# Performance work log

Measured on AMD Instinct MI355X. Metric: run time of the kernel, lower is better.

The kernel has to match this reference:

```python
import jax, jax.numpy as jnp
import numpy as np
from jax.scipy.linalg import expm

DIM = 2048        # state dimension (init arg `dim`)
M_STEPS = 8192    # kernel length (init arg `timestamp`)
DELTA = 0.01      # ZOH step size (init arg `delta`)
STAB = 1e-3       # stabilizer added to A before inversion (matches torch code)


def setup_inputs() -> dict:
    key = jax.random.key(0)
    k1, k2, k3 = jax.random.split(key, 3)
    # Match the torch init scaling so matrix_exp/inv stay well-conditioned.
    A = jnp.eye(DIM, dtype=jnp.float32) * -0.01 \
        + jax.random.normal(k1, (DIM, DIM), dtype=jnp.float32) * 0.001
    B = jax.random.normal(k2, (DIM, 1), dtype=jnp.float32) * 0.01
    C = jax.random.normal(k3, (1, DIM), dtype=jnp.float32) * 0.01
    return {"A": A, "B": B, "C": C, "M": M_STEPS}


def reference(A, B, C, M):
    dim = A.shape[0]
    I = jnp.eye(dim, dtype=A.dtype)
    # --- ZOH discretization (torch._zoh_discretize) ---
    A_bar = expm(DELTA * A)                         # [dim, dim]
    A_inv = jnp.linalg.inv(A + STAB * I)            # [dim, dim]
    B_bar = A_inv @ (A_bar - I) @ (DELTA * B)       # [dim, 1]

    # --- kernel power iteration (torch._compute_K_bar) ---
    # K[t] = C @ A_bar^t @ B_bar. Since B_bar is a vector, the serial
    # matrix-power loop reduces to M sequential matvecs (same math).
    def step(x, _):
        term = (C @ x)[0, 0]        # scalar K_t
        return A_bar @ x, term      # advance state: A_bar^{t+1} B_bar

    _, terms = jax.lax.scan(step, B_bar, None, length=M)  # [M]
    K_bar = terms[::-1][None, :]    # flip along time, shape [1, M]
    return K_bar
```

## Files before the change

kernel.cpp:

```cpp
#include <hip/hip_runtime.h>
#include <hip/hip_bf16.h>


#define DIMN 2048
#define MSTEPS 8192
#define RSPLIT 91
#define NN ((size_t)DIMN * DIMN)
#define NBLK 32
#define ALD 36
#define GJP 65
#define TBM 128

typedef short short8 __attribute__((ext_vector_type(8)));
typedef float f32x4 __attribute__((ext_vector_type(4)));

__device__ inline void split1(float x, unsigned short& h, unsigned short& l)
{
  __hip_bfloat16 b = __float2bfloat16(x);
  h = *reinterpret_cast<unsigned short*>(&b);
  float r = x - __bfloat162float(b);
  __hip_bfloat16 b2 = __float2bfloat16(r);
  l = *reinterpret_cast<unsigned short*>(&b2);
}

__global__ __launch_bounds__(256)
void k_combine4(float* out,
                const float* i1, float c1, const float* i2, float c2,
                const float* i3, float c3, const float* i4, float c4,
                float dval)
{
  const int total = DIMN * DIMN;
  for (int idx = blockIdx.x * 256 + threadIdx.x; idx < total; idx += gridDim.x * 256) {
    float v = 0.f;
    if (i1) v = fmaf(c1, i1[idx], v);
    if (i2) v = fmaf(c2, i2[idx], v);
    if (i3) v = fmaf(c3, i3[idx], v);
    if (i4) v = fmaf(c4, i4[idx], v);
    if ((idx >> 11) == (idx & 2047)) v += dval;
    out[idx] = v;
  }
}

__global__ __launch_bounds__(256)
void k_fill64(const float* __restrict__ A, double* __restrict__ M)
{
  const int total = DIMN * DIMN;
  for (int idx = blockIdx.x * 256 + threadIdx.x; idx < total; idx += gridDim.x * 256) {
    double v = (double)A[idx];
    if ((idx >> 11) == (idx & 2047)) v += 1e-3;
    M[idx] = v;
  }
}

__global__ __launch_bounds__(256)
void k_split(const float* __restrict__ in, unsigned short* __restrict__ hi,
             unsigned short* __restrict__ lo)
{
  const int i4 = blockIdx.x * 256 + threadIdx.x;
  const float4 v = ((const float4*)in)[i4];
  ushort4 h, l;
  split1(v.x, h.x, l.x); split1(v.y, h.y, l.y);
  split1(v.z, h.z, l.z); split1(v.w, h.w, l.w);
  ((ushort4*)hi)[i4] = h;
  ((ushort4*)lo)[i4] = l;
}

__global__ __launch_bounds__(256)
void k_splitboth(const float* __restrict__ in,
                 unsigned short* __restrict__ hi, unsigned short* __restrict__ lo,
                 unsigned short* __restrict__ hiT, unsigned short* __restrict__ loT)
{
  __shared__ float t[32][33];
  const int bx = blockIdx.x * 32, by = blockIdx.y * 32;
  const int lx = threadIdx.x, ly = threadIdx.y;
  for (int dy = 0; dy < 32; dy += 8) {
    const size_t o = (size_t)(by + ly + dy) * DIMN + bx + lx;
    const float v = in[o];
    t[ly + dy][lx] = v;
    unsigned short h, l;
    split1(v, h, l);
    hi[o] = h; lo[o] = l;
  }
  __syncthreads();
  for (int dy = 0; dy < 32; dy += 8) {
    const size_t o = (size_t)(bx + ly + dy) * DIMN + by + lx;
    unsigned short h, l;
    split1(t[lx][ly + dy], h, l);
    hiT[o] = h; loT[o] = l;
  }
}

__global__ __launch_bounds__(256)
void k_combsplitT(const float* __restrict__ i1, float c1,
                  const float* __restrict__ i2, float c2,
                  unsigned short* __restrict__ hiT, unsigned short* __restrict__ loT)
{
  __shared__ float t[32][33];
  const int bx = blockIdx.x * 32, by = blockIdx.y * 32;
  const int lx = threadIdx.x, ly = threadIdx.y;
  for (int dy = 0; dy < 32; dy += 8) {
    const size_t o = (size_t)(by + ly + dy) * DIMN + bx + lx;
    t[ly + dy][lx] = fmaf(c1, i1[o], c2 * i2[o]);
  }
  __syncthreads();
  for (int dy = 0; dy < 32; dy += 8) {
    const size_t o = (size_t)(bx + ly + dy) * DIMN + by + lx;
    unsigned short h, l;
    split1(t[lx][ly + dy], h, l);
    hiT[o] = h; loT[o] = l;
  }
}

__global__ __launch_bounds__(256)
void k_gemm3(const unsigned short* __restrict__ Ahg, const unsigned short* __restrict__ Alg,
             const unsigned short* __restrict__ Bhg, const unsigned short* __restrict__ Blg,
             float* __restrict__ C, float alpha,
             const float* E1, float c1, const float* E2, float c2)
{
  __shared__ unsigned short sAh[128 * ALD];
  __shared__ unsigned short sAl[128 * ALD];
  __shared__ unsigned short sBh[128 * ALD];
  __shared__ unsigned short sBl[128 * ALD];
  const int tid = threadIdx.x;
  const int wid = tid >> 6, lane = tid & 63;
  const int lr = lane & 15, lg = lane >> 4;
  const int wm = wid >> 1, wn = wid & 1;
  const int bid0 = blockIdx.y * 16 + blockIdx.x;
  const int bids = (bid0 & 7) * 32 + (bid0 >> 3);
  const int brow = (bids >> 4) * 128, bcol = (bids & 15) * 128;
  const int sr = tid >> 1, sh = (tid & 1) * 16;

  const unsigned short* gAh = Ahg + (size_t)(brow + sr) * DIMN + sh;
  const unsigned short* gAl = Alg + (size_t)(brow + sr) * DIMN + sh;
  const unsigned short* gBh = Bhg + (size_t)(bcol + sr) * DIMN + sh;
  const unsigned short* gBl = Blg + (size_t)(bcol + sr) * DIMN + sh;

  f32x4 acc[4][4];
#pragma unroll
  for (int mf = 0; mf < 4; ++mf)
#pragma unroll
    for (int nf = 0; nf < 4; ++nf) acc[mf][nf] = (f32x4){0.f, 0.f, 0.f, 0.f};

  uint4 pa0 = *(const uint4*)gAh;      uint4 pa1 = *(const uint4*)(gAh + 8);
  uint4 pb0 = *(const uint4*)gAl;      uint4 pb1 = *(const uint4*)(gAl + 8);
  uint4 pc0 = *(const uint4*)gBh;      uint4 pc1 = *(const uint4*)(gBh + 8);
  uint4 pd0 = *(const uint4*)gBl;      uint4 pd1 = *(const uint4*)(gBl + 8);

  const int nk = DIMN / 32;
  for (int kt = 0; kt < nk; ++kt) {
    *(uint4*)&sAh[sr * ALD + sh] = pa0;  *(uint4*)&sAh[sr * ALD + sh + 8] = pa1;
    *(uint4*)&sAl[sr * ALD + sh] = pb0;  *(uint4*)&sAl[sr * ALD + sh + 8] = pb1;
    *(uint4*)&sBh[sr * ALD + sh] = pc0;  *(uint4*)&sBh[sr * ALD + sh + 8] = pc1;
    *(uint4*)&sBl[sr * ALD + sh] = pd0;  *(uint4*)&sBl[sr * ALD + sh + 8] = pd1;
    __syncthreads();
    if (kt + 1 < nk) {
      const int o = (kt + 1) * 32;
      pa0 = *(const uint4*)(gAh + o);  pa1 = *(const uint4*)(gAh + o + 8);
      pb0 = *(const uint4*)(gAl + o);  pb1 = *(const uint4*)(gAl + o + 8);
      pc0 = *(const uint4*)(gBh + o);  pc1 = *(const uint4*)(gBh + o + 8);
      pd0 = *(const uint4*)(gBl + o);  pd1 = *(const uint4*)(gBl + o + 8);
    }
    short8 bh[4], bl[4];
#pragma unroll
    for (int nf = 0; nf < 4; ++nf) {
      const int br = 64 * wn + 16 * nf + lr;
      bh[nf] = *(const short8*)&sBh[br * ALD + lg * 8];
      bl[nf] = *(const short8*)&sBl[br * ALD + lg * 8];
    }
#pragma unroll
    for (int mf = 0; mf < 4; ++mf) {
      const int ar = 64 * wm + 16 * mf + lr;
      const short8 ah = *(const short8*)&sAh[ar * ALD + lg * 8];
      const short8 al = *(const short8*)&sAl[ar * ALD + lg * 8];
#pragma unroll
      for (int nf = 0; nf < 4; ++nf) {
        acc[mf][nf] = __builtin_amdgcn_mfma_f32_16x16x32_bf16(ah, bh[nf], acc[mf][nf], 0, 0, 0);
        acc[mf][nf] = __builtin_amdgcn_mfma_f32_16x16x32_bf16(ah, bl[nf], acc[mf][nf], 0, 0, 0);
        acc[mf][nf] = __builtin_amdgcn_mfma_f32_16x16x32_bf16(al, bh[nf], acc[mf][nf], 0, 0, 0);
      }
    }
    __syncthreads();
  }
#pragma unroll
  for (int mf = 0; mf < 4; ++mf) {
#pragma unroll
    for (int nf = 0; nf < 4; ++nf) {
      const int col = bcol + 64 * wn + 16 * nf + lr;
#pragma unroll
      for (int i = 0; i < 4; ++i) {
        const int row = brow + 64 * wm + 16 * mf + 4 * lg + i;
        float v = alpha * acc[mf][nf][i];
        if (E1) v = fmaf(c1, E1[(size_t)row * DIMN + col], v);
        if (E2) v = fmaf(c2, E2[(size_t)row * DIMN + col], v);
        C[(size_t)row * DIMN + col] = v;
      }
    }
  }
}

__global__ __launch_bounds__(256, 1)
void k_dtrail(const double* __restrict__ Cp, const double* __restrict__ Rp,
              double* __restrict__ M)
{
  __shared__ double As[8][TBM];
  __shared__ double Bs[8][TBM];
  const int tid = threadIdx.x;
  const int bid0 = blockIdx.y * 16 + blockIdx.x;
  const int bids = (bid0 & 7) * 32 + (bid0 >> 3);
  const int brow = (bids >> 4) * TBM, bcol = (bids & 15) * TBM;
  const int tx = tid & 15, ty = tid >> 4;

  const int ar = tid >> 1, ac = (tid & 1) * 4;
  const int br = tid >> 5, bc = (tid & 31) * 4;

  const double* Ap = Cp + (size_t)(brow + ar) * 64 + ac;
  const double* Bp = Rp + (size_t)br * DIMN + (bcol + bc);

  double4 aPre = *(const double4*)Ap;
  double4 bPre = *(const double4*)Bp;

  double acc[8][8];
#pragma unroll
  for (int i = 0; i < 8; ++i)
#pragma unroll
    for (int j = 0; j < 8; ++j) acc[i][j] = 0.0;

  for (int kt = 0; kt < 8; ++kt) {
    As[ac + 0][ar] = aPre.x; As[ac + 1][ar] = aPre.y;
    As[ac + 2][ar] = aPre.z; As[ac + 3][ar] = aPre.w;
    *(double4*)&Bs[br][bc] = bPre;
    __syncthreads();
    if (kt + 1 < 8) {
      aPre = *(const double4*)(Ap + (kt + 1) * 8);
      bPre = *(const double4*)(Bp + (size_t)(kt + 1) * 8 * DIMN);
    }
#pragma unroll
    for (int kk = 0; kk < 8; ++kk) {
      double a[8], b[8];
#pragma unroll
      for (int i = 0; i < 8; ++i) a[i] = As[kk][ty * 8 + i];
#pragma unroll
      for (int j = 0; j < 8; ++j) b[j] = Bs[kk][tx * 8 + j];
#pragma unroll
      for (int i = 0; i < 8; ++i)
#pragma unroll
        for (int j = 0; j < 8; ++j)
          acc[i][j] = fma(a[i], b[j], acc[i][j]);
    }
    __syncthreads();
  }
#pragma unroll
  for (int i = 0; i < 8; ++i) {
    const size_t ro = (size_t)(brow + ty * 8 + i) * DIMN + bcol + tx * 8;
    double4 m0 = *(const double4*)&M[ro];
    double4 m1 = *(const double4*)&M[ro + 4];
    m0.x -= acc[i][0]; m0.y -= acc[i][1]; m0.z -= acc[i][2]; m0.w -= acc[i][3];
    m1.x -= acc[i][4]; m1.y -= acc[i][5]; m1.z -= acc[i][6]; m1.w -= acc[i][7];
    *(double4*)&M[ro] = m0;
    *(double4*)&M[ro + 4] = m1;
  }
}

__global__ __launch_bounds__(256)
void k_gj64(const double* __restrict__ M, int ldm, double* __restrict__ W, int ldw)
{
  __shared__ double a[128][GJP];
  const int tid = threadIdx.x;
  const int rg = tid & 7;
  const int cg = tid >> 3;

  for (int idx = tid; idx < 64 * 64; idx += 256) {
    const int r = idx >> 6, c = idx & 63;
    a[c][r] = M[(size_t)r * ldm + c];
    a[64 + c][r] = (r == c) ? 1.0 : 0.0;
  }
  __syncthreads();

  for (int p = 0; p < 64; ++p) {
    const double rpv = 1.0 / a[p][p];
    const int c0 = p + 1 + cg;
    const int c1 = c0 + 32;
    const double prs0 = a[c0][p] * rpv;
    const double prs1 = a[c1][p] * rpv;
    double colp[8];
#pragma unroll
    for (int k = 0; k < 4; ++k) {
      const double2 t2 = *(const double2*)&a[p][rg * 8 + 2 * k];
      colp[2 * k] = t2.x; colp[2 * k + 1] = t2.y;
    }
    __syncthreads();
#pragma unroll
    for (int k = 0; k < 8; ++k) {
      const int r = rg * 8 + k;
      const bool isp = (r == p);
      const double v0 = a[c0][r];
      const double v1 = a[c1][r];
      a[c0][r] = isp ? prs0 : fma(-colp[k], prs0, v0);
      a[c1][r] = isp ? prs1 : fma(-colp[k], prs1, v1);
    }
    __syncthreads();
  }

  for (int idx = tid; idx < 64 * 64; idx += 256) {
    const int r = idx >> 6, c = idx & 63;
    W[(size_t)r * ldw + c] = a[64 + c][r];
  }
}

#define DBM 64
#define DBK 8
__global__ __launch_bounds__(256)
void k_stagefix(const double* __restrict__ Dinv, double* __restrict__ M,
                double* __restrict__ Rpan, double* __restrict__ Cpan, int p)
{
  const int blk = blockIdx.x;
  const int tid = threadIdx.x;
  if (blk >= 32) {
    const int idx = (blk - 32) * 256 + tid;
    const int i = idx >> 6, k = idx & 63;
    const bool inP = (i >> 6) == p;
    const size_t mo = (size_t)i * DIMN + p * 64 + k;
    double v = 0.0;
    if (!inP) { v = M[mo]; M[mo] = 0.0; }
    Cpan[idx] = v;
    return;
  }
  __shared__ double As[DBK][DBM];
  __shared__ double Bs[DBK][DBM];
  const double* Mrow = M + (size_t)p * 64 * DIMN;
  const int tx = tid & 15, ty = tid >> 4;
  const int bcol = blk * DBM;

  const int arow = tid >> 2, ac0 = (tid & 3) * 2;
  const int brw  = tid >> 5, bc0 = (tid & 31) * 2;

  const double* Aptr = Dinv + (size_t)arow * 64 + ac0;
  const double* Bptr = Mrow + (size_t)brw * DIMN + (bcol + bc0);

  double2 aPre = *(const double2*)Aptr;
  double2 bPre = *(const double2*)Bptr;

  double acc[4][4];
#pragma unroll
  for (int i = 0; i < 4; ++i)
#pragma unroll
    for (int j = 0; j < 4; ++j) acc[i][j] = 0.0;

  for (int kt = 0; kt < 8; ++kt) {
    As[ac0 + 0][arow] = aPre.x;
    As[ac0 + 1][arow] = aPre.y;
    Bs[brw][bc0 + 0] = bPre.x;
    Bs[brw][bc0 + 1] = bPre.y;
    __syncthreads();
    if (kt + 1 < 8) {
      aPre = *(const double2*)(Aptr + (size_t)(kt + 1) * DBK);
      bPre = *(const double2*)(Bptr + (size_t)(kt + 1) * DBK * DIMN);
    }
#pragma unroll
    for (int kk = 0; kk < DBK; ++kk) {
      double a[4], b[4];
#pragma unroll
      for (int i = 0; i < 4; ++i) a[i] = As[kk][ty * 4 + i];
#pragma unroll
      for (int j = 0; j < 4; ++j) b[j] = Bs[kk][tx * 4 + j];
#pragma unroll
      for (int i = 0; i < 4; ++i)
#pragma unroll
        for (int j = 0; j < 4; ++j)
          acc[i][j] = fma(a[i], b[j], acc[i][j]);
    }
    __syncthreads();
  }
  const bool pivcol = (bcol >> 6) == p;
#pragma unroll
  for (int i = 0; i < 4; ++i) {
    const int gi = ty * 4 + i;
#pragma unroll
    for (int j = 0; j < 4; ++j) {
      const int gj = bcol + tx * 4 + j;
      double v = pivcol ? Dinv[(size_t)gi * 64 + (gj & 63)] : acc[i][j];
      Rpan[(size_t)gi * DIMN + gj] = v;
      M[(size_t)(p * 64 + gi) * DIMN + gj] = v;
    }
  }
}

__global__ __launch_bounds__(256)
void k_mv(const float* __restrict__ Mat, const double* __restrict__ vin,
          double* vout, const double* vadd, double alpha)
{
  const int lane = threadIdx.x & 63;
  const int row = blockIdx.x * 4 + (threadIdx.x >> 6);
  const float* mrow = Mat + (size_t)row * DIMN;
  double acc = 0.0;
  for (int p = 0; p < DIMN; p += 256) {
    const float4 m = *(const float4*)&mrow[p + lane * 4];
    const double* vp = &vin[p + lane * 4];
    acc += (double)m.x * vp[0] + (double)m.y * vp[1] + (double)m.z * vp[2] + (double)m.w * vp[3];
  }
  for (int off = 32; off; off >>= 1) acc += __shfl_down(acc, off);
  if (lane == 0) vout[row] = alpha * acc + (vadd ? vadd[row] : 0.0);
}

__global__ __launch_bounds__(256)
void k_mv64(const double* __restrict__ W, const double* __restrict__ vin,
            double* vout, const double* vadd, double alpha)
{
  const int lane = threadIdx.x & 63;
  const int row = blockIdx.x * 4 + (threadIdx.x >> 6);
  const double* mrow = W + (size_t)row * DIMN;
  double acc = 0.0;
  for (int p = 0; p < DIMN; p += 256) {
    const int idx = p + lane * 4;
    const double2 m0 = *(const double2*)&mrow[idx];
    const double2 m1 = *(const double2*)&mrow[idx + 2];
    acc += m0.x * vin[idx] + m0.y * vin[idx + 1] + m1.x * vin[idx + 2] + m1.y * vin[idx + 3];
  }
  for (int off = 32; off; off >>= 1) acc += __shfl_down(acc, off);
  if (lane == 0) vout[row] = alpha * acc + (vadd ? vadd[row] : 0.0);
}

__global__ __launch_bounds__(256)
void k_mvres(const float* __restrict__ A, const double* __restrict__ x,
             const double* __restrict__ y, double* r)
{
  const int lane = threadIdx.x & 63;
  const int row = blockIdx.x * 4 + (threadIdx.x >> 6);
  const float* mrow = A + (size_t)row * DIMN;
  double acc = 0.0;
  for (int p = 0; p < DIMN; p += 256) {
    const float4 m = *(const float4*)&mrow[p + lane * 4];
    const double* vp = &x[p + lane * 4];
    acc += (double)m.x * vp[0] + (double)m.y * vp[1] + (double)m.z * vp[2] + (double)m.w * vp[3];
  }
  for (int off = 32; off; off >>= 1) acc += __shfl_down(acc, off);
  if (lane == 0) r[row] = y[row] - acc - 1e-3 * x[row];
}

__global__ __launch_bounds__(256)
void k_transpose(const float* __restrict__ in, float* __restrict__ out)
{
  __shared__ float t[32][33];
  const int bx = blockIdx.x * 32, by = blockIdx.y * 32;
  const int lx = threadIdx.x, ly = threadIdx.y;
  for (int dy = 0; dy < 32; dy += 8)
    t[ly + dy][lx] = in[(size_t)(by + ly + dy) * DIMN + bx + lx];
  __syncthreads();
  for (int dy = 0; dy < 32; dy += 8)
    out[(size_t)(bx + ly + dy) * DIMN + by + lx] = t[lx][ly + dy];
}

__global__ __launch_bounds__(256)
void k_chain(const float* __restrict__ E, const float* __restrict__ vin, float* __restrict__ vout,
             const float* __restrict__ ERT, const float* __restrict__ uin, float* __restrict__ uout)
{
  const int lane = threadIdx.x & 63;
  const int w = threadIdx.x >> 6;
  const int b = blockIdx.x;
  const float* mrow; const float* xin; float* xout; int row;
  if (b < 512) { row = b * 4 + w; mrow = E + (size_t)row * DIMN; xin = vin; xout = vout; }
  else { row = (b - 512) * 4 + w; mrow = ERT + (size_t)row * DIMN; xin = uin; xout = uout; }
  float acc = 0.f;
  for (int p = 0; p < DIMN; p += 256) {
    const float4 m = *(const float4*)&mrow[p + lane * 4];
    const float* vp = &xin[p + lane * 4];
    acc = fmaf(m.x, vp[0], acc);
    acc = fmaf(m.y, vp[1], acc);
    acc = fmaf(m.z, vp[2], acc);
    acc = fmaf(m.w, vp[3], acc);
  }
  for (int off = 32; off; off >>= 1) acc += __shfl_down(acc, off);
  if (lane == 0) xout[row] = xin[row] + acc;
}

__global__ __launch_bounds__(256)
void k_chainb(const float* __restrict__ E8, const float* __restrict__ Vin,
              float* __restrict__ Vout, int do_v,
              const float* __restrict__ A4T, const float* __restrict__ Uin,
              float* __restrict__ Uout)
{
  const int lane = threadIdx.x & 63;
  const int w = threadIdx.x >> 6;
  const int b = blockIdx.x;
  if (b < 512) {
    if (!do_v) return;
    const int row = b * 4 + w;
    const float* mrow = E8 + (size_t)row * DIMN;
    float acc[8];
#pragma unroll
    for (int r = 0; r < 8; ++r) acc[r] = 0.f;
    for (int p = 0; p < DIMN; p += 256) {
      const float4 m = *(const float4*)&mrow[p + lane * 4];
#pragma unroll
      for (int r = 0; r < 8; ++r) {
        const float4 v = *(const float4*)&Vin[(size_t)r * DIMN + p + lane * 4];
        acc[r] = fmaf(m.x, v.x, acc[r]);
        acc[r] = fmaf(m.y, v.y, acc[r]);
        acc[r] = fmaf(m.z, v.z, acc[r]);
        acc[r] = fmaf(m.w, v.w, acc[r]);
      }
    }
#pragma unroll
    for (int r = 0; r < 8; ++r) {
      float a = acc[r];
      for (int off = 32; off; off >>= 1) a += __shfl_down(a, off);
      if (lane == 0) Vout[(size_t)r * DIMN + row] = Vin[(size_t)r * DIMN + row] + a;
    }
  } else {
    const int row = (b - 512) * 4 + w;
    const float* mrow = A4T + (size_t)row * DIMN;
    float acc[4];
#pragma unroll
    for (int r = 0; r < 4; ++r) acc[r] = 0.f;
    for (int p = 0; p < DIMN; p += 256) {
      const float4 m = *(const float4*)&mrow[p + lane * 4];
#pragma unroll
      for (int r = 0; r < 4; ++r) {
        const float4 v = *(const float4*)&Uin[(size_t)r * DIMN + p + lane * 4];
        acc[r] = fmaf(m.x, v.x, acc[r]);
        acc[r] = fmaf(m.y, v.y, acc[r]);
        acc[r] = fmaf(m.z, v.z, acc[r]);
        acc[r] = fmaf(m.w, v.w, acc[r]);
      }
    }
#pragma unroll
    for (int r = 0; r < 4; ++r) {
      float a = acc[r];
      for (int off = 32; off; off >>= 1) a += __shfl_down(a, off);
      if (lane == 0) Uout[(size_t)r * DIMN + row] = Uin[(size_t)r * DIMN + row] + a;
    }
  }
}

__global__ __launch_bounds__(256)
void k_terms(const float* __restrict__ U, const float* __restrict__ V, float* __restrict__ out)
{
  const int lane = threadIdx.x & 63;
  const int t = blockIdx.x * 4 + (threadIdx.x >> 6);
  const int j = t / RSPLIT, i = t - j * RSPLIT;
  const float* u = U + (size_t)j * DIMN;
  const float* v = V + (size_t)i * DIMN;
  float acc = 0.f;
  for (int p = 0; p < DIMN; p += 256) {
    const float4 a4 = *(const float4*)&u[p + lane * 4];
    const float4 b4 = *(const float4*)&v[p + lane * 4];
    acc = fmaf(a4.x, b4.x, acc); acc = fmaf(a4.y, b4.y, acc);
    acc = fmaf(a4.z, b4.z, acc); acc = fmaf(a4.w, b4.w, acc);
  }
  for (int off = 32; off; off >>= 1) acc += __shfl_down(acc, off);
  if (lane == 0) out[MSTEPS - 1 - t] = acc;
}

__global__ void k_vecinit(const float* __restrict__ B, double* __restrict__ b64,
                          const float* __restrict__ Cv, float* __restrict__ U0)
{
  const int i = blockIdx.x * 256 + threadIdx.x;
  if (i < DIMN) { b64[i] = 0.01 * (double)B[i]; U0[i] = Cv[i]; }
}
__global__ void k_v0(const double* __restrict__ x64, float* __restrict__ V0)
{
  const int i = blockIdx.x * 256 + threadIdx.x;
  if (i < DIMN) V0[i] = (float)x64[i];
}

extern "C" void kernel_launch(void* const* d_in, const int* in_sizes, int n_in,
                              void* d_out, int out_size, void* d_ws, size_t ws_size,
                              hipStream_t stream)
{
  const float* dA = (const float*)d_in[0];
  const float* dB = (const float*)d_in[1];
  const float* dC = (const float*)d_in[2];
  float* out = (float*)d_out;

  float* fb = (float*)d_ws;
  float* Ebuf = fb;
  float* t1 = fb + NN;
  float* t2 = t1 + NN;
  float* t3 = t2 + NN;
  float* t4 = t3 + NN;
  float* t5 = t4 + NN;
  double* M64 = (double*)t1;
  double* scr64 = (double*)(fb + 6 * NN);
  double* Dinv = scr64;
  double* Cpan = Dinv + 64 * 64;
  double* Rpan = Cpan + (size_t)DIMN * 64;
  double* y64 = Rpan + (size_t)DIMN * 64;
  double* x64 = y64 + DIMN;
  double* r64 = x64 + DIMN;
  double* b64 = r64 + DIMN;
  float* V  = (float*)(b64 + DIMN);
  float* Uc = V + (size_t)96 * DIMN;

  const size_t needed = 6 * NN * 4
                        + (64 * 64 + 2 * (size_t)DIMN * 64 + 4 * (size_t)DIMN) * 8
                        + (size_t)(96 + 92) * DIMN * 4;
  if (ws_size < needed) return;

  const float* NUL = nullptr;
  dim3 cb(256), cg(2048);

  unsigned short* Ah  = (unsigned short*)t4;   unsigned short* Al  = Ah + NN;
  unsigned short* Ath = (unsigned short*)Ebuf; unsigned short* Atl = Ath + NN;
  unsigned short* Y2h = (unsigned short*)t1;   unsigned short* Y2l = Y2h + NN;
  unsigned short* Hth = (unsigned short*)t2;   unsigned short* Htl = Hth + NN;

  k_splitboth<<<dim3(64, 64), dim3(32, 8), 0, stream>>>(dA, Ah, Al, Ath, Atl);
  k_gemm3<<<dim3(16, 16), cb, 0, stream>>>(Ah, Al, Ath, Atl, t3, 0.8281f,
                                           NUL, 0.f, NUL, 0.f);
  k_combine4<<<cg, cb, 0, stream>>>(Ebuf, t3, (float)(5e-5 / 0.8281), dA, 0.01f,
                                    NUL, 0, NUL, 0, 0.f);

  k_fill64<<<cg, cb, 0, stream>>>(dA, M64);
  for (int p = 0; p < NBLK; ++p) {
    double* Mrow = M64 + (size_t)p * 64 * DIMN;
    k_gj64<<<dim3(1), cb, 0, stream>>>(Mrow + p * 64, DIMN, Dinv, 64);
    k_stagefix<<<dim3(544), cb, 0, stream>>>(Dinv, M64, Rpan, Cpan, p);
    k_dtrail<<<dim3(16, 16), cb, 0, stream>>>(Cpan, Rpan, M64);
  }

  k_vecinit<<<dim3(8), cb, 0, stream>>>(dB, b64, dC, Uc);
  k_mv<<<dim3(512), cb, 0, stream>>>(Ebuf, b64, y64, (const double*)nullptr, 1.0);
  k_mv64<<<dim3(512), cb, 0, stream>>>(M64, y64, x64, (const double*)nullptr, 1.0);
  k_mvres<<<dim3(512), cb, 0, stream>>>(dA, x64, y64, r64);
  k_mv64<<<dim3(512), cb, 0, stream>>>(M64, r64, x64, x64, 1.0);
  k_v0<<<dim3(8), cb, 0, stream>>>(x64, V);

  k_split<<<dim3(4096), cb, 0, stream>>>(t3, Y2h, Y2l);
  k_combsplitT<<<dim3(64, 64), dim3(32, 8), 0, stream>>>(dA, 0.91f / 6.f,
                                                         t3, 1.f / 24.f, Hth, Htl);
  k_gemm3<<<dim3(16, 16), cb, 0, stream>>>(Y2h, Y2l, Hth, Htl, t4, 1.f,
                                           t3, 0.5f, dA, 0.91f);
  k_transpose<<<dim3(64, 64), dim3(32, 8), 0, stream>>>(t4, t5);
  k_combsplitT<<<dim3(64, 64), dim3(32, 8), 0, stream>>>(dA, 3.64f / 6.f,
                                                         t3, 16.f / 24.f, Hth, Htl);
  k_gemm3<<<dim3(16, 16), cb, 0, stream>>>(Y2h, Y2l, Hth, Htl, t4, 16.f,
                                           t3, 8.f, dA, 3.64f);
  k_combine4<<<cg, cb, 0, stream>>>(t1, dA, 0.08f, t3, (float)(0.0032 / 0.8281),
                                    NUL, 0, NUL, 0, 0.f);
  k_transpose<<<dim3(64, 64), dim3(32, 8), 0, stream>>>(t4, t3);

  for (int s = 0; s < 7; ++s) {
    k_chain<<<dim3(1024), cb, 0, stream>>>(Ebuf, V + (size_t)s * DIMN, V + (size_t)(s + 1) * DIMN,
                                           t5, Uc + (size_t)s * DIMN, Uc + (size_t)(s + 1) * DIMN);
  }
  for (int i = 0; i < 22; ++i) {
    k_chainb<<<dim3(1024), cb, 0, stream>>>(
        t1, V + (size_t)(8 * i) * DIMN, V + (size_t)(8 * i + 8) * DIMN, (i < 11) ? 1 : 0,
        t3, Uc + (size_t)(4 * i) * DIMN, Uc + (size_t)(4 * i + 4) * DIMN);
  }
  k_terms<<<dim3(2048), cb, 0, stream>>>(Uc, V, out);
}
```

Before: 4.425 ms.

## Fuse diagonal-block Gauss-Jordan inverse into trailing update and fold combine into GEMM epilogue

Replaces the per-stage sequence of single-block inversion kernel, panel fix and 128-tile fp64 trailing update with a 64-tile trailing update. The block owning the next diagonal tile also inverts it in shared memory, which removes one serialized single-block launch per stage of the blocked inversion. The separate combine pass that builds Ebuf is folded into the first GEMM epilogue through an extra output, and the split buffers move so they no longer alias Ebuf. The cost is smaller tiles with a 1024-block grid, and one block doing a serial 64-step elimination at the end of the trailing kernel, which may leave that kernel waiting on a long tail block.

```diff
diff --git a/kernel.cpp b/kernel.cpp
--- a/kernel.cpp
+++ b/kernel.cpp
@@ -9,7 +9,6 @@
 #define NBLK 32
 #define ALD 36
 #define GJP 65
-#define TBM 128
 
 typedef short short8 __attribute__((ext_vector_type(8)));
 typedef float f32x4 __attribute__((ext_vector_type(4)));
@@ -115,7 +114,8 @@
 void k_gemm3(const unsigned short* __restrict__ Ahg, const unsigned short* __restrict__ Alg,
              const unsigned short* __restrict__ Bhg, const unsigned short* __restrict__ Blg,
              float* __restrict__ C, float alpha,
-             const float* E1, float c1, const float* E2, float c2)
+             const float* E1, float c1, const float* E2, float c2,
+             const float* Ab, float* O2, float o2ab, float o2a)
 {
   __shared__ unsigned short sAh[128 * ALD];
   __shared__ unsigned short sAl[128 * ALD];
@@ -189,75 +189,15 @@
 #pragma unroll
       for (int i = 0; i < 4; ++i) {
         const int row = brow + 64 * wm + 16 * mf + 4 * lg + i;
-        float v = alpha * acc[mf][nf][i];
-        if (E1) v = fmaf(c1, E1[(size_t)row * DIMN + col], v);
-        if (E2) v = fmaf(c2, E2[(size_t)row * DIMN + col], v);
-        C[(size_t)row * DIMN + col] = v;
+        const size_t off = (size_t)row * DIMN + col;
+        const float va = alpha * acc[mf][nf][i];
+        float v = va;
+        if (E1) v = fmaf(c1, E1[off], v);
+        if (E2) v = fmaf(c2, E2[off], v);
+        C[off] = v;
+        if (O2) O2[off] = fmaf(o2ab, va, o2a * Ab[off]);
       }
     }
-  }
-}
-
-__global__ __launch_bounds__(256, 1)
-void k_dtrail(const double* __restrict__ Cp, const double* __restrict__ Rp,
-              double* __restrict__ M)
-{
-  __shared__ double As[8][TBM];
-  __shared__ double Bs[8][TBM];
-  const int tid = threadIdx.x;
-  const int bid0 = blockIdx.y * 16 + blockIdx.x;
-  const int bids = (bid0 & 7) * 32 + (bid0 >> 3);
-  const int brow = (bids >> 4) * TBM, bcol = (bids & 15) * TBM;
-  const int tx = tid & 15, ty = tid >> 4;
-
-  const int ar = tid >> 1, ac = (tid & 1) * 4;
-  const int br = tid >> 5, bc = (tid & 31) * 4;
-
-  const double* Ap = Cp + (size_t)(brow + ar) * 64 + ac;
-  const double* Bp = Rp + (size_t)br * DIMN + (bcol + bc);
-
-  double4 aPre = *(const double4*)Ap;
-  double4 bPre = *(const double4*)Bp;
-
-  double acc[8][8];
-#pragma unroll
-  for (int i = 0; i < 8; ++i)
-#pragma unroll
-    for (int j = 0; j < 8; ++j) acc[i][j] = 0.0;
-
-  for (int kt = 0; kt < 8; ++kt) {
-    As[ac + 0][ar] = aPre.x; As[ac + 1][ar] = aPre.y;
-    As[ac + 2][ar] = aPre.z; As[ac + 3][ar] = aPre.w;
-    *(double4*)&Bs[br][bc] = bPre;
-    __syncthreads();
-    if (kt + 1 < 8) {
-      aPre = *(const double4*)(Ap + (kt + 1) * 8);
-      bPre = *(const double4*)(Bp + (size_t)(kt + 1) * 8 * DIMN);
-    }
-#pragma unroll
-    for (int kk = 0; kk < 8; ++kk) {
-      double a[8], b[8];
-#pragma unroll
-      for (int i = 0; i < 8; ++i) a[i] = As[kk][ty * 8 + i];
-#pragma unroll
-      for (int j = 0; j < 8; ++j) b[j] = Bs[kk][tx * 8 + j];
-#pragma unroll
-      for (int i = 0; i < 8; ++i)
-#pragma unroll
-        for (int j = 0; j < 8; ++j)
-          acc[i][j] = fma(a[i], b[j], acc[i][j]);
-    }
-    __syncthreads();
-  }
-#pragma unroll
-  for (int i = 0; i < 8; ++i) {
-    const size_t ro = (size_t)(brow + ty * 8 + i) * DIMN + bcol + tx * 8;
-    double4 m0 = *(const double4*)&M[ro];
-    double4 m1 = *(const double4*)&M[ro + 4];
-    m0.x -= acc[i][0]; m0.y -= acc[i][1]; m0.z -= acc[i][2]; m0.w -= acc[i][3];
-    m1.x -= acc[i][4]; m1.y -= acc[i][5]; m1.z -= acc[i][6]; m1.w -= acc[i][7];
-    *(double4*)&M[ro] = m0;
-    *(double4*)&M[ro + 4] = m1;
   }
 }
 
@@ -304,6 +244,117 @@
   for (int idx = tid; idx < 64 * 64; idx += 256) {
     const int r = idx >> 6, c = idx & 63;
     W[(size_t)r * ldw + c] = a[64 + c][r];
+  }
+}
+
+__global__ __launch_bounds__(256)
+void k_ftrail(const double* __restrict__ Cp, const double* __restrict__ Rp,
+              double* __restrict__ M, double* __restrict__ Dinv, int sgj, int do_gj)
+{
+  __shared__ double As[8][66];
+  __shared__ double Bs[8][66];
+  __shared__ double aj[64][65];
+  const int tid = threadIdx.x;
+  const int bid0 = blockIdx.y * 32 + blockIdx.x;
+  const int dd = sgj * 32 + sgj;
+  int t = bid0;
+  if (do_gj) { if (bid0 == 0) t = dd; else if (bid0 == dd) t = 0; }
+  const int tr = t >> 5, tc = t & 31;
+  const int brow = tr * 64, bcol = tc * 64;
+  const int tx = tid & 15, ty = tid >> 4;
+
+  const int arow = tid >> 2, ac0 = (tid & 3) * 2;
+  const int brw  = tid >> 5, bc0 = (tid & 31) * 2;
+
+  const double* Ap = Cp + (size_t)(brow + arow) * 64 + ac0;
+  const double* Bp = Rp + (size_t)brw * DIMN + (bcol + bc0);
+  double2 aPre = *(const double2*)Ap;
+  double2 bPre = *(const double2*)Bp;
+
+  double acc[4][4];
+#pragma unroll
+  for (int i = 0; i < 4; ++i)
+#pragma unroll
+    for (int j = 0; j < 4; ++j) acc[i][j] = 0.0;
+
+  for (int kt = 0; kt < 8; ++kt) {
+    As[ac0 + 0][arow] = aPre.x;
+    As[ac0 + 1][arow] = aPre.y;
+    Bs[brw][bc0 + 0] = bPre.x;
+    Bs[brw][bc0 + 1] = bPre.y;
+    __syncthreads();
+    if (kt + 1 < 8) {
+      aPre = *(const double2*)(Ap + (kt + 1) * 8);
+      bPre = *(const double2*)(Bp + (size_t)(kt + 1) * 8 * DIMN);
+    }
+#pragma unroll
+    for (int kk = 0; kk < 8; ++kk) {
+      double a[4], b[4];
+#pragma unroll
+      for (int i = 0; i < 4; ++i) a[i] = As[kk][ty * 4 + i];
+#pragma unroll
+      for (int j = 0; j < 4; ++j) b[j] = Bs[kk][tx * 4 + j];
+#pragma unroll
+      for (int i = 0; i < 4; ++i)
+#pragma unroll
+        for (int j = 0; j < 4; ++j)
+          acc[i][j] = fma(a[i], b[j], acc[i][j]);
+    }
+    __syncthreads();
+  }
+
+  double vout[4][4];
+#pragma unroll
+  for (int i = 0; i < 4; ++i) {
+#pragma unroll
+    for (int j = 0; j < 4; ++j) {
+      const size_t mo = (size_t)(brow + ty * 4 + i) * DIMN + bcol + tx * 4 + j;
+      const double v = M[mo] - acc[i][j];
+      vout[i][j] = v;
+      M[mo] = v;
+    }
+  }
+
+  if (!(do_gj && tr == sgj && tc == sgj)) return;
+
+#pragma unroll
+  for (int i = 0; i < 4; ++i)
+#pragma unroll
+    for (int j = 0; j < 4; ++j)
+      aj[tx * 4 + j][ty * 4 + i] = vout[i][j];
+  __syncthreads();
+
+  const int rg = tid & 7;
+  const int cg = tid >> 3;
+  const int c0 = cg, c1 = cg + 32;
+  for (int p = 0; p < 64; ++p) {
+    const double d = 1.0 / aj[p][p];
+    const double r0d = aj[c0][p] * d;
+    const double r1d = aj[c1][p] * d;
+    double colp[8];
+#pragma unroll
+    for (int k = 0; k < 4; ++k) {
+      const double2 t2 = *(const double2*)&aj[p][rg * 8 + 2 * k];
+      colp[2 * k] = t2.x; colp[2 * k + 1] = t2.y;
+    }
+    __syncthreads();
+#pragma unroll
+    for (int k = 0; k < 8; ++k) {
+      const int r = rg * 8 + k;
+      double nv0;
+      if (r == p) nv0 = (c0 == p) ? d : r0d;
+      else nv0 = (c0 == p) ? (-colp[k] * d) : fma(-colp[k], r0d, aj[c0][r]);
+      aj[c0][r] = nv0;
+      double nv1;
+      if (r == p) nv1 = (c1 == p) ? d : r1d;
+      else nv1 = (c1 == p) ? (-colp[k] * d) : fma(-colp[k], r1d, aj[c1][r]);
+      aj[c1][r] = nv1;
+    }
+    __syncthreads();
+  }
+  for (int idx = tid; idx < 64 * 64; idx += 256) {
+    const int r = idx >> 6, c = idx & 63;
+    Dinv[idx] = aj[c][r];
   }
 }
 
@@ -597,25 +648,25 @@
   if (ws_size < needed) return;
 
   const float* NUL = nullptr;
+  float* NULo = nullptr;
   dim3 cb(256), cg(2048);
 
   unsigned short* Ah  = (unsigned short*)t4;   unsigned short* Al  = Ah + NN;
-  unsigned short* Ath = (unsigned short*)Ebuf; unsigned short* Atl = Ath + NN;
+  unsigned short* Ath = (unsigned short*)t5;   unsigned short* Atl = Ath + NN;
   unsigned short* Y2h = (unsigned short*)t1;   unsigned short* Y2l = Y2h + NN;
   unsigned short* Hth = (unsigned short*)t2;   unsigned short* Htl = Hth + NN;
 
   k_splitboth<<<dim3(64, 64), dim3(32, 8), 0, stream>>>(dA, Ah, Al, Ath, Atl);
   k_gemm3<<<dim3(16, 16), cb, 0, stream>>>(Ah, Al, Ath, Atl, t3, 0.8281f,
-                                           NUL, 0.f, NUL, 0.f);
-  k_combine4<<<cg, cb, 0, stream>>>(Ebuf, t3, (float)(5e-5 / 0.8281), dA, 0.01f,
-                                    NUL, 0, NUL, 0, 0.f);
+                                           NUL, 0.f, NUL, 0.f,
+                                           dA, Ebuf, (float)(5e-5 / 0.8281), 0.01f);
 
   k_fill64<<<cg, cb, 0, stream>>>(dA, M64);
-  for (int p = 0; p < NBLK; ++p) {
-    double* Mrow = M64 + (size_t)p * 64 * DIMN;
-    k_gj64<<<dim3(1), cb, 0, stream>>>(Mrow + p * 64, DIMN, Dinv, 64);
-    k_stagefix<<<dim3(544), cb, 0, stream>>>(Dinv, M64, Rpan, Cpan, p);
-    k_dtrail<<<dim3(16, 16), cb, 0, stream>>>(Cpan, Rpan, M64);
+  k_gj64<<<dim3(1), cb, 0, stream>>>(M64, DIMN, Dinv, 64);
+  for (int s = 0; s < NBLK; ++s) {
+    k_stagefix<<<dim3(544), cb, 0, stream>>>(Dinv, M64, Rpan, Cpan, s);
+    k_ftrail<<<dim3(32, 32), cb, 0, stream>>>(Cpan, Rpan, M64, Dinv, s + 1,
+                                              (s < NBLK - 1) ? 1 : 0);
   }
 
   k_vecinit<<<dim3(8), cb, 0, stream>>>(dB, b64, dC, Uc);
@@ -629,12 +680,14 @@
   k_combsplitT<<<dim3(64, 64), dim3(32, 8), 0, stream>>>(dA, 0.91f / 6.f,
                                                          t3, 1.f / 24.f, Hth, Htl);
   k_gemm3<<<dim3(16, 16), cb, 0, stream>>>(Y2h, Y2l, Hth, Htl, t4, 1.f,
-                                           t3, 0.5f, dA, 0.91f);
+                                           t3, 0.5f, dA, 0.91f,
+                                           NUL, NULo, 0.f, 0.f);
   k_transpose<<<dim3(64, 64), dim3(32, 8), 0, stream>>>(t4, t5);
   k_combsplitT<<<dim3(64, 64), dim3(32, 8), 0, stream>>>(dA, 3.64f / 6.f,
                                                          t3, 16.f / 24.f, Hth, Htl);
   k_gemm3<<<dim3(16, 16), cb, 0, stream>>>(Y2h, Y2l, Hth, Htl, t4, 16.f,
-                                           t3, 8.f, dA, 3.64f);
+                                           t3, 8.f, dA, 3.64f,
+                                           NUL, NULo, 0.f, 0.f);
   k_combine4<<<cg, cb, 0, stream>>>(t1, dA, 0.08f, t3, (float)(0.0032 / 0.8281),
                                     NUL, 0, NUL, 0, 0.f);
   k_transpose<<<dim3(64, 64), dim3(32, 8), 0, stream>>>(t4, t3);
```

Result: faster. 4.269 ms (-3.5%).
